# Kernel tuning notes

Measured on AMD Instinct MI355X. Metric: run time of the kernel, lower is better.

Reference implementation:

```python
import jax, jax.numpy as jnp
import numpy as np

N = 8192
NFEAT = 64
OUT = 64


def setup_inputs() -> dict:
    key = jax.random.key(0)
    ks = jax.random.split(key, 7)
    A_stack = jax.random.uniform(ks[0], (N, N, 5), dtype=jnp.float32)
    feature = jax.random.normal(ks[1], (N, NFEAT), dtype=jnp.float32)
    weight_b = jax.random.uniform(ks[2], (5, 1), dtype=jnp.float32) * 0.1
    stdv1 = 1.0 / np.sqrt(OUT)
    W1 = jax.random.uniform(ks[3], (NFEAT, OUT), dtype=jnp.float32, minval=-stdv1, maxval=stdv1)
    b1 = jax.random.uniform(ks[4], (OUT,), dtype=jnp.float32, minval=-stdv1, maxval=stdv1)
    W2 = jax.random.uniform(ks[5], (OUT, OUT), dtype=jnp.float32, minval=-stdv1, maxval=stdv1)
    b2 = jax.random.uniform(ks[6], (OUT,), dtype=jnp.float32, minval=-stdv1, maxval=stdv1)
    return {"A_stack": A_stack, "feature": feature, "weight_b": weight_b,
            "W1": W1, "b1": b1, "W2": W2, "b2": b2}


def reference(A_stack, feature, weight_b, W1, b1, W2, b2):
    # Multiplex relation aggregation: weighted sum of 5 adjacency layers, then symmetrize.
    temp = jnp.einsum('ijk,kl->ij', A_stack, weight_b)  # [N, N]
    final_A = temp + temp.T
    # GCN layer 1: spmm(adj, X @ W1) + b1
    U1 = final_A @ (feature @ W1) + b1
    # GCN layer 2
    U2 = final_A @ (U1 @ W2) + b2
    return (U1 + U2) * 0.5
```

## Files before the change

kernel.cpp:

```cpp
#include <hip/hip_runtime.h>
#include <hip/hip_bf16.h>


#define NN 8192

typedef __attribute__((ext_vector_type(8))) short short8;
typedef __attribute__((ext_vector_type(8))) unsigned short u16x8;
typedef __attribute__((ext_vector_type(4))) unsigned short u16x4;
typedef __attribute__((ext_vector_type(4))) float f32x4;

static __device__ __forceinline__ unsigned short f2bf(float f) {
    unsigned u = __float_as_uint(f);
    u += 0x7FFFu + ((u >> 16) & 1u);
    return (unsigned short)(u >> 16);
}

__global__ __launch_bounds__(256) void k_sym_build(
        const float* __restrict__ A, const float* __restrict__ wb,
        unsigned short* __restrict__ S) {
    __shared__ float Tt[64 * 65];

    int b = blockIdx.x;
    double disc = 66049.0 - 8.0 * (double)b;
    int bi = (int)((257.0 - sqrt(disc)) * 0.5);
    if (bi < 0) bi = 0; if (bi > 127) bi = 127;
    while (bi < 127 && (bi + 1) * (257 - (bi + 1)) / 2 <= b) ++bi;
    while (bi > 0 && bi * (257 - bi) / 2 > b) --bi;
    int bj = bi + (b - bi * (257 - bi) / 2);

    const float w0 = wb[0], w1 = wb[1], w2 = wb[2], w3 = wb[3], w4 = wb[4];
    int t = threadIdx.x;
    int qc = t & 15;
    int r0 = t >> 4;

    float t1[4][4];
    #pragma unroll
    for (int e = 0; e < 4; ++e) {
        int r = r0 + 16 * e;
        {
            const f32x4* p = (const f32x4*)(A +
                ((long long)(bi * 64 + r) * NN + bj * 64 + 4 * qc) * 5);
            f32x4 f0 = p[0], f1 = p[1], f2 = p[2], f3 = p[3], f4 = p[4];
            t1[e][0] = f0[0]*w0 + f0[1]*w1 + f0[2]*w2 + f0[3]*w3 + f1[0]*w4;
            t1[e][1] = f1[1]*w0 + f1[2]*w1 + f1[3]*w2 + f2[0]*w3 + f2[1]*w4;
            t1[e][2] = f2[2]*w0 + f2[3]*w1 + f3[0]*w2 + f3[1]*w3 + f3[2]*w4;
            t1[e][3] = f3[3]*w0 + f4[0]*w1 + f4[1]*w2 + f4[2]*w3 + f4[3]*w4;
        }
        {
            const f32x4* p = (const f32x4*)(A +
                ((long long)(bj * 64 + r) * NN + bi * 64 + 4 * qc) * 5);
            f32x4 f0 = p[0], f1 = p[1], f2 = p[2], f3 = p[3], f4 = p[4];
            Tt[r * 65 + 4*qc + 0] = f0[0]*w0 + f0[1]*w1 + f0[2]*w2 + f0[3]*w3 + f1[0]*w4;
            Tt[r * 65 + 4*qc + 1] = f1[1]*w0 + f1[2]*w1 + f1[3]*w2 + f2[0]*w3 + f2[1]*w4;
            Tt[r * 65 + 4*qc + 2] = f2[2]*w0 + f2[3]*w1 + f3[0]*w2 + f3[1]*w3 + f3[2]*w4;
            Tt[r * 65 + 4*qc + 3] = f3[3]*w0 + f4[0]*w1 + f4[1]*w2 + f4[2]*w3 + f4[3]*w4;
        }
    }
    __syncthreads();
    float sv[4][4];
    #pragma unroll
    for (int e = 0; e < 4; ++e) {
        int r = r0 + 16 * e;
        u16x4 o;
        #pragma unroll
        for (int q = 0; q < 4; ++q) {
            float v = t1[e][q] + Tt[(4*qc + q) * 65 + r];
            sv[e][q] = v;
            o[q] = f2bf(v);
        }
        *(u16x4*)(S + (long long)(bi * 64 + r) * NN + bj * 64 + 4 * qc) = o;
    }
    __syncthreads();
    #pragma unroll
    for (int e = 0; e < 4; ++e) {
        int r = r0 + 16 * e;
        #pragma unroll
        for (int q = 0; q < 4; ++q) Tt[r * 65 + 4*qc + q] = sv[e][q];
    }
    __syncthreads();
    if (bi != bj) {
        #pragma unroll
        for (int e = 0; e < 4; ++e) {
            int r = r0 + 16 * e;
            u16x4 o;
            #pragma unroll
            for (int q = 0; q < 4; ++q) o[q] = f2bf(Tt[(4*qc + q) * 65 + r]);
            *(u16x4*)(S + (long long)(bj * 64 + r) * NN + bi * 64 + 4 * qc) = o;
        }
    }
}

__global__ __launch_bounds__(256) void k_small_gemm_t(
        const float* __restrict__ X, const float* __restrict__ W,
        unsigned short* __restrict__ Yt) {
    __shared__ float Ys[64 * 65];
    int t = threadIdx.x, lane = t & 63, w = t >> 6;
    float wcol[64];
    #pragma unroll
    for (int k = 0; k < 64; ++k) wcol[k] = W[k * 64 + lane];
    int r0 = blockIdx.x * 64;
    for (int rr = 0; rr < 16; ++rr) {
        const f32x4* x = (const f32x4*)(X + (long long)(r0 + w * 16 + rr) * 64);
        float acc = 0.f;
        #pragma unroll
        for (int k4 = 0; k4 < 16; ++k4) {
            f32x4 xv = x[k4];
            acc += xv[0]*wcol[4*k4] + xv[1]*wcol[4*k4+1]
                 + xv[2]*wcol[4*k4+2] + xv[3]*wcol[4*k4+3];
        }
        Ys[lane * 65 + w * 16 + rr] = acc;
    }
    __syncthreads();
    int c = t >> 2, j0 = (t & 3) * 16;
    u16x8 o0, o1;
    #pragma unroll
    for (int q = 0; q < 8; ++q) {
        o0[q] = f2bf(Ys[c * 65 + j0 + q]);
        o1[q] = f2bf(Ys[c * 65 + j0 + 8 + q]);
    }
    *(u16x8*)(Yt + (long long)c * NN + r0 + j0) = o0;
    *(u16x8*)(Yt + (long long)c * NN + r0 + j0 + 8) = o1;
}

template<int FINAL>
__global__ __launch_bounds__(256) void k_gemm_skinny(
        const unsigned short* __restrict__ S,
        const unsigned short* __restrict__ Ht,
        const float* __restrict__ bias,
        const float* __restrict__ U1,
        float* __restrict__ Y) {
    __shared__ float red[4][16][64];
    int t = threadIdx.x;
    int lane = t & 63, w = t >> 6;
    int i0 = blockIdx.x * 16;
    int r = lane & 15, kg = lane >> 4;

    const unsigned short* aRow = S + (long long)(i0 + r) * NN + kg * 8;
    const unsigned short* bRow = Ht + (long long)r * NN + kg * 8;
    f32x4 acc0 = {0,0,0,0}, acc1 = {0,0,0,0}, acc2 = {0,0,0,0}, acc3 = {0,0,0,0};

    int j0 = w * 2048;
    for (int jt = j0; jt < j0 + 2048; jt += 128) {
        #pragma unroll
        for (int kk = 0; kk < 4; ++kk) {
            int off = jt + kk * 32;
            short8 a   = *(const short8*)(aRow + off);
            short8 bb0 = *(const short8*)(bRow + off);
            short8 bb1 = *(const short8*)(bRow + 16 * NN + off);
            short8 bb2 = *(const short8*)(bRow + 32 * NN + off);
            short8 bb3 = *(const short8*)(bRow + 48 * NN + off);
            acc0 = __builtin_amdgcn_mfma_f32_16x16x32_bf16(a, bb0, acc0, 0, 0, 0);
            acc1 = __builtin_amdgcn_mfma_f32_16x16x32_bf16(a, bb1, acc1, 0, 0, 0);
            acc2 = __builtin_amdgcn_mfma_f32_16x16x32_bf16(a, bb2, acc2, 0, 0, 0);
            acc3 = __builtin_amdgcn_mfma_f32_16x16x32_bf16(a, bb3, acc3, 0, 0, 0);
        }
    }
    #pragma unroll
    for (int rr = 0; rr < 4; ++rr) {
        red[w][kg * 4 + rr][r]      = acc0[rr];
        red[w][kg * 4 + rr][16 + r] = acc1[rr];
        red[w][kg * 4 + rr][32 + r] = acc2[rr];
        red[w][kg * 4 + rr][48 + r] = acc3[rr];
    }
    __syncthreads();
    #pragma unroll
    for (int e = 0; e < 4; ++e) {
        int idx = t + e * 256;
        int m = idx >> 6, c = idx & 63;
        float v = red[0][m][c] + red[1][m][c] + red[2][m][c] + red[3][m][c] + bias[c];
        long long gi = (long long)(i0 + m) * 64 + c;
        if (FINAL) v = 0.5f * (U1[gi] + v);
        Y[gi] = v;
    }
}

extern "C" void kernel_launch(void* const* d_in, const int* in_sizes, int n_in,
                              void* d_out, int out_size, void* d_ws, size_t ws_size,
                              hipStream_t stream) {
    const float* A    = (const float*)d_in[0];
    const float* feat = (const float*)d_in[1];
    const float* wb   = (const float*)d_in[2];
    const float* W1   = (const float*)d_in[3];
    const float* b1   = (const float*)d_in[4];
    const float* W2   = (const float*)d_in[5];
    const float* b2   = (const float*)d_in[6];
    float* out = (float*)d_out;

    const size_t szS = (size_t)NN * NN * 2;
    const size_t szH = (size_t)64 * NN * 2;
    char* p = (char*)d_ws;
    unsigned short* S   = (unsigned short*)p;
    unsigned short* H1t = (unsigned short*)(p + szS);
    unsigned short* H2t = (unsigned short*)(p + szS + szH);
    float*          U1  = (float*)(p + szS + 2 * szH);

    k_sym_build<<<8256, 256, 0, stream>>>(A, wb, S);
    k_small_gemm_t<<<128, 256, 0, stream>>>(feat, W1, H1t);
    k_gemm_skinny<0><<<512, 256, 0, stream>>>(S, H1t, b1, nullptr, U1);
    k_small_gemm_t<<<128, 256, 0, stream>>>(U1, W2, H2t);
    k_gemm_skinny<1><<<512, 256, 0, stream>>>(S, H2t, b2, U1, out);
}
```

Before: 501.8 us.

## Stage skinny GEMM tiles through LDS with async double-buffered loads

The skinny GEMM kernel now loads each 128-wide K slice of S and Ht into swizzled LDS buffers with global_load_lds and double-buffers them. All four waves share the same A tile, and each wave computes one 16-column slice of the output over the full K range instead of splitting K across waves. This removes the redundant per-wave global reads of Ht, the four-way cross-wave reduction and its shared buffer. The cost is a block-wide barrier per K step and only one MFMA accumulator chain per wave, which gives less instruction-level parallelism.

```diff
diff --git a/kernel.cpp b/kernel.cpp
--- a/kernel.cpp
+++ b/kernel.cpp
@@ -14,6 +14,10 @@
     u += 0x7FFFu + ((u >> 16) & 1u);
     return (unsigned short)(u >> 16);
 }
+
+#define GL16(gsrc, ldst) __builtin_amdgcn_global_load_lds( \
+    (const __attribute__((address_space(1))) void*)(gsrc), \
+    (__attribute__((address_space(3))) void*)(ldst), 16, 0, 0)
 
 __global__ __launch_bounds__(256) void k_sym_build(
         const float* __restrict__ A, const float* __restrict__ wb,
@@ -129,46 +133,64 @@
         const float* __restrict__ bias,
         const float* __restrict__ U1,
         float* __restrict__ Y) {
-    __shared__ float red[4][16][64];
-    int t = threadIdx.x;
-    int lane = t & 63, w = t >> 6;
+    __shared__ unsigned short Ts[2][16 * 128];
+    __shared__ unsigned short Hs[2][64 * 128];
+    int t = threadIdx.x, lane = t & 63, w = t >> 6;
     int i0 = blockIdx.x * 16;
     int r = lane & 15, kg = lane >> 4;
 
-    const unsigned short* aRow = S + (long long)(i0 + r) * NN + kg * 8;
-    const unsigned short* bRow = Ht + (long long)r * NN + kg * 8;
-    f32x4 acc0 = {0,0,0,0}, acc1 = {0,0,0,0}, acc2 = {0,0,0,0}, acc3 = {0,0,0,0};
-
-    int j0 = w * 2048;
-    for (int jt = j0; jt < j0 + 2048; jt += 128) {
+    int srow = t >> 4, sc = t & 15;
+    int sbyte = (sc * 16) ^ ((srow & 7) << 4);
+    const unsigned short* aSrc = S + (long long)(i0 + srow) * NN + (sbyte >> 1);
+    const unsigned short* hSrc = Ht + (long long)srow * NN + (sbyte >> 1);
+    char* tsDst0 = (char*)&Ts[0][0] + t * 16;
+    char* tsDst1 = (char*)&Ts[1][0] + t * 16;
+    char* hsDst0 = (char*)&Hs[0][0] + t * 16;
+    char* hsDst1 = (char*)&Hs[1][0] + t * 16;
+
+    f32x4 acc = {0.f, 0.f, 0.f, 0.f};
+
+    GL16(aSrc, tsDst0);
+    #pragma unroll
+    for (int q = 0; q < 4; ++q)
+        GL16(hSrc + (long long)q * 16 * NN, hsDst0 + q * 4096);
+    __syncthreads();
+
+    int cur = 0;
+    for (int jt = 0; jt < NN; jt += 128) {
+        if (jt + 128 < NN) {
+            if (cur == 0) {
+                GL16(aSrc + jt + 128, tsDst1);
+                #pragma unroll
+                for (int q = 0; q < 4; ++q)
+                    GL16(hSrc + (long long)q * 16 * NN + jt + 128, hsDst1 + q * 4096);
+            } else {
+                GL16(aSrc + jt + 128, tsDst0);
+                #pragma unroll
+                for (int q = 0; q < 4; ++q)
+                    GL16(hSrc + (long long)q * 16 * NN + jt + 128, hsDst0 + q * 4096);
+            }
+        }
+        const char* tsB = (const char*)&Ts[cur][0];
+        const char* hsB = (const char*)&Hs[cur][0];
+        int hr = w * 16 + r;
         #pragma unroll
         for (int kk = 0; kk < 4; ++kk) {
-            int off = jt + kk * 32;
-            short8 a   = *(const short8*)(aRow + off);
-            short8 bb0 = *(const short8*)(bRow + off);
-            short8 bb1 = *(const short8*)(bRow + 16 * NN + off);
-            short8 bb2 = *(const short8*)(bRow + 32 * NN + off);
-            short8 bb3 = *(const short8*)(bRow + 48 * NN + off);
-            acc0 = __builtin_amdgcn_mfma_f32_16x16x32_bf16(a, bb0, acc0, 0, 0, 0);
-            acc1 = __builtin_amdgcn_mfma_f32_16x16x32_bf16(a, bb1, acc1, 0, 0, 0);
-            acc2 = __builtin_amdgcn_mfma_f32_16x16x32_bf16(a, bb2, acc2, 0, 0, 0);
-            acc3 = __builtin_amdgcn_mfma_f32_16x16x32_bf16(a, bb3, acc3, 0, 0, 0);
-        }
-    }
+            int xo = kk * 64 + kg * 16;
+            short8 a = *(const short8*)(tsB + r * 256 + (xo ^ ((r & 7) << 4)));
+            short8 bb = *(const short8*)(hsB + hr * 256 + (xo ^ ((r & 7) << 4)));
+            acc = __builtin_amdgcn_mfma_f32_16x16x32_bf16(a, bb, acc, 0, 0, 0);
+        }
+        __syncthreads();
+        cur ^= 1;
+    }
+
+    int f = w * 16 + r;
+    float bv = bias[f];
     #pragma unroll
     for (int rr = 0; rr < 4; ++rr) {
-        red[w][kg * 4 + rr][r]      = acc0[rr];
-        red[w][kg * 4 + rr][16 + r] = acc1[rr];
-        red[w][kg * 4 + rr][32 + r] = acc2[rr];
-        red[w][kg * 4 + rr][48 + r] = acc3[rr];
-    }
-    __syncthreads();
-    #pragma unroll
-    for (int e = 0; e < 4; ++e) {
-        int idx = t + e * 256;
-        int m = idx >> 6, c = idx & 63;
-        float v = red[0][m][c] + red[1][m][c] + red[2][m][c] + red[3][m][c] + bias[c];
-        long long gi = (long long)(i0 + m) * 64 + c;
+        long long gi = (long long)(i0 + kg * 4 + rr) * 64 + f;
+        float v = acc[rr] + bv;
         if (FINAL) v = 0.5f * (U1[gi] + v);
         Y[gi] = v;
     }
```

After: 445.3 us. 11.3% less time.
